# Kernel tuning notes

Measured on AMD Instinct MI355X. Metric: run time of the kernel, lower is better.

Reference implementation:

```python
import jax, jax.numpy as jnp
import numpy as np


def setup_inputs() -> dict:
    key = jax.random.key(0)
    k1, k2 = jax.random.split(key)
    B, C, H, W = 32, 8, 256, 256
    inp = jax.random.normal(k1, (B, C, H, W), dtype=jnp.float32)
    tgt = jax.random.uniform(k2, (B, C, H, W), dtype=jnp.float32)
    return {"input": inp, "target": tgt}


def reference(input, target):
    B, C, H, W = input.shape
    # normalized coordinate grids: (index+1)/size, as in the original loops
    x_grid = (jnp.arange(W, dtype=input.dtype) + 1.0) / W          # [W]
    y_grid = (jnp.arange(H, dtype=input.dtype) + 1.0) / H          # [H]

    # per-(b,c) softmax over the flattened heatmap (DSNT)
    p = jax.nn.softmax(input.reshape(B, C, H * W), axis=-1).reshape(B, C, H, W)
    pred_x = jnp.einsum('bchw,w->bc', p, x_grid)                   # [B, C]
    pred_y = jnp.einsum('bchw,h->bc', p, y_grid)                   # [B, C]

    # ground-truth coords from argmax of target heatmap
    idx = jnp.argmax(target.reshape(B, C, H * W), axis=-1)         # [B, C] int
    true_x = ((idx % W) + 1).astype(input.dtype) / W
    true_y = ((idx // W) + 1).astype(input.dtype) / H

    ed = jnp.sqrt((true_x - pred_x) ** 2 + (true_y - pred_y) ** 2)  # [B, C]
    # original sums over all (batch, channel) pairs, divides by batch size only
    return jnp.sum(ed) / B
```

## Files before the change

### kernel.cpp

```cpp
#include <hip/hip_runtime.h>
#include <math.h>


constexpr int HW    = 256 * 256;
constexpr int BLOCK = 1024;
constexpr int WAVES = BLOCK / 64;
constexpr int ITERS = (HW / 4) / BLOCK;

__global__ __launch_bounds__(BLOCK) void dsnt_loss_kernel(
        const float* __restrict__ input,
        const float* __restrict__ target,
        float* __restrict__ out)
{
    const int bc = blockIdx.x;
    const float4* __restrict__ in4 =
        reinterpret_cast<const float4*>(input) + (size_t)bc * (HW / 4);
    const float4* __restrict__ tg4 =
        reinterpret_cast<const float4*>(target) + (size_t)bc * (HW / 4);
    const int tid = threadIdx.x;

    float s = 0.f, sx = 0.f, sy = 0.f;
    float bv = -INFINITY;
    int   bi = 0x7FFFFFFF;

    #pragma unroll
    for (int i = 0; i < ITERS; ++i) {
        const int j = tid + i * BLOCK;
        const float4 v = in4[j];
        const float4 t = tg4[j];
        const int f = 4 * j;
        const float y  = (float)((f >> 8) + 1) * (1.0f / 256.0f);
        const float x0 = (float)((f & 255) + 1) * (1.0f / 256.0f);

        const float e0 = __expf(v.x);
        const float e1 = __expf(v.y);
        const float e2 = __expf(v.z);
        const float e3 = __expf(v.w);
        const float es = (e0 + e1) + (e2 + e3);
        s  += es;
        sy += es * y;
        sx += e0 * x0
            + e1 * (x0 + 1.0f / 256.0f)
            + e2 * (x0 + 2.0f / 256.0f)
            + e3 * (x0 + 3.0f / 256.0f);

        if (t.x > bv) { bv = t.x; bi = f; }
        if (t.y > bv) { bv = t.y; bi = f + 1; }
        if (t.z > bv) { bv = t.z; bi = f + 2; }
        if (t.w > bv) { bv = t.w; bi = f + 3; }
    }

    #pragma unroll
    for (int off = 32; off > 0; off >>= 1) {
        s  += __shfl_down(s, off);
        sx += __shfl_down(sx, off);
        sy += __shfl_down(sy, off);
        const float ov = __shfl_down(bv, off);
        const int   oi = __shfl_down(bi, off);
        if (ov > bv || (ov == bv && oi < bi)) { bv = ov; bi = oi; }
    }

    __shared__ float ls[WAVES], lsx[WAVES], lsy[WAVES], lbv[WAVES];
    __shared__ int   lbi[WAVES];
    const int wave = tid >> 6;
    const int lane = tid & 63;
    if (lane == 0) {
        ls[wave]  = s;
        lsx[wave] = sx;
        lsy[wave] = sy;
        lbv[wave] = bv;
        lbi[wave] = bi;
    }
    __syncthreads();

    if (tid == 0) {
        #pragma unroll
        for (int wv = 1; wv < WAVES; ++wv) {
            s  += ls[wv];
            sx += lsx[wv];
            sy += lsy[wv];
            if (lbv[wv] > bv || (lbv[wv] == bv && lbi[wv] < bi)) {
                bv = lbv[wv];
                bi = lbi[wv];
            }
        }
        const float px = sx / s;
        const float py = sy / s;
        const float tx = (float)((bi & 255) + 1) * (1.0f / 256.0f);
        const float ty = (float)((bi >> 8) + 1) * (1.0f / 256.0f);
        const float dx = tx - px;
        const float dy = ty - py;
        const float ed = sqrtf(dx * dx + dy * dy);
        atomicAdd(out, ed * (1.0f / 32.0f));
    }
}

extern "C" void kernel_launch(void* const* d_in, const int* in_sizes, int n_in,
                              void* d_out, int out_size, void* d_ws, size_t ws_size,
                              hipStream_t stream) {
    const float* input  = (const float*)d_in[0];
    const float* target = (const float*)d_in[1];
    float* out = (float*)d_out;

    const int n_maps = in_sizes[0] / HW;

    hipMemsetAsync(out, 0, sizeof(float), stream);
    dsnt_loss_kernel<<<n_maps, BLOCK, 0, stream>>>(input, target, out);
}
```

Measured before the change: 146.6 us.

## Split each heatmap across multiple blocks with atomic partial reduction and final kernel

Each (b,c) map is now processed by 8 blocks of 512 threads instead of one 1024-thread block, giving 2048 blocks rather than 256 so the 256 CUs fill more evenly and more loads stay in flight. Partial sums go to a workspace through float atomics, and the argmax is merged with a packed 64-bit atomicMax key that breaks ties toward the lower index. A second small kernel finishes the per-map loss and the sum. This adds a memset, a second launch and atomic traffic, and float atomics make the sum order nondeterministic.

```diff
diff --git a/kernel.cpp b/kernel.cpp
--- a/kernel.cpp
+++ b/kernel.cpp
@@ -2,22 +2,33 @@
 #include <math.h>
 
 
-constexpr int HW    = 256 * 256;
-constexpr int BLOCK = 1024;
-constexpr int WAVES = BLOCK / 64;
-constexpr int ITERS = (HW / 4) / BLOCK;
+constexpr int HW     = 256 * 256;
+constexpr int SPLIT  = 8;
+constexpr int BLOCK  = 512;
+constexpr int WAVES  = BLOCK / 64;
+constexpr int CHUNK4 = (HW / 4) / SPLIT;
+constexpr int ITERS  = CHUNK4 / BLOCK;
 
-__global__ __launch_bounds__(BLOCK) void dsnt_loss_kernel(
+struct Ws {
+    unsigned long long key[256];
+    float s[256];
+    float sx[256];
+    float sy[256];
+};
+
+__global__ __launch_bounds__(BLOCK) void dsnt_partial_kernel(
         const float* __restrict__ input,
         const float* __restrict__ target,
-        float* __restrict__ out)
+        Ws* __restrict__ ws)
 {
-    const int bc = blockIdx.x;
-    const float4* __restrict__ in4 =
-        reinterpret_cast<const float4*>(input) + (size_t)bc * (HW / 4);
-    const float4* __restrict__ tg4 =
-        reinterpret_cast<const float4*>(target) + (size_t)bc * (HW / 4);
-    const int tid = threadIdx.x;
+    const int chunk = blockIdx.x;
+    const int bc    = blockIdx.y;
+    const int tid   = threadIdx.x;
+
+    const size_t base4 = (size_t)bc * (HW / 4) + (size_t)chunk * CHUNK4;
+    const float4* __restrict__ in4 = reinterpret_cast<const float4*>(input)  + base4;
+    const float4* __restrict__ tg4 = reinterpret_cast<const float4*>(target) + base4;
+    const int fbase = chunk * (HW / SPLIT);
 
     float s = 0.f, sx = 0.f, sy = 0.f;
     float bv = -INFINITY;
@@ -28,7 +39,7 @@
         const int j = tid + i * BLOCK;
         const float4 v = in4[j];
         const float4 t = tg4[j];
-        const int f = 4 * j;
+        const int f = fbase + 4 * j;
         const float y  = (float)((f >> 8) + 1) * (1.0f / 256.0f);
         const float x0 = (float)((f & 255) + 1) * (1.0f / 256.0f);
 
@@ -65,11 +76,8 @@
     const int wave = tid >> 6;
     const int lane = tid & 63;
     if (lane == 0) {
-        ls[wave]  = s;
-        lsx[wave] = sx;
-        lsy[wave] = sy;
-        lbv[wave] = bv;
-        lbi[wave] = bi;
+        ls[wave] = s; lsx[wave] = sx; lsy[wave] = sy;
+        lbv[wave] = bv; lbi[wave] = bi;
     }
     __syncthreads();
 
@@ -80,18 +88,46 @@
             sx += lsx[wv];
             sy += lsy[wv];
             if (lbv[wv] > bv || (lbv[wv] == bv && lbi[wv] < bi)) {
-                bv = lbv[wv];
-                bi = lbi[wv];
+                bv = lbv[wv]; bi = lbi[wv];
             }
         }
-        const float px = sx / s;
-        const float py = sy / s;
+        atomicAdd(&ws->s[bc],  s);
+        atomicAdd(&ws->sx[bc], sx);
+        atomicAdd(&ws->sy[bc], sy);
+        const unsigned long long key =
+            ((unsigned long long)__float_as_uint(bv) << 32) |
+            (unsigned long long)(~(unsigned int)bi);
+        atomicMax(&ws->key[bc], key);
+    }
+}
+
+__global__ __launch_bounds__(256) void dsnt_final_kernel(
+        const Ws* __restrict__ ws,
+        float* __restrict__ out,
+        int n_maps)
+{
+    const int tid = threadIdx.x;
+    float ed = 0.f;
+    if (tid < n_maps) {
+        const float s  = ws->s[tid];
+        const float px = ws->sx[tid] / s;
+        const float py = ws->sy[tid] / s;
+        const unsigned int inv_idx = (unsigned int)(ws->key[tid] & 0xFFFFFFFFu);
+        const int bi = (int)(~inv_idx);
         const float tx = (float)((bi & 255) + 1) * (1.0f / 256.0f);
         const float ty = (float)((bi >> 8) + 1) * (1.0f / 256.0f);
         const float dx = tx - px;
         const float dy = ty - py;
-        const float ed = sqrtf(dx * dx + dy * dy);
-        atomicAdd(out, ed * (1.0f / 32.0f));
+        ed = sqrtf(dx * dx + dy * dy);
+    }
+    #pragma unroll
+    for (int off = 32; off > 0; off >>= 1) ed += __shfl_down(ed, off);
+    __shared__ float lw[4];
+    const int wave = tid >> 6;
+    if ((tid & 63) == 0) lw[wave] = ed;
+    __syncthreads();
+    if (tid == 0) {
+        out[0] = (lw[0] + lw[1] + lw[2] + lw[3]) * (1.0f / 32.0f);
     }
 }
 
@@ -101,9 +137,11 @@
     const float* input  = (const float*)d_in[0];
     const float* target = (const float*)d_in[1];
     float* out = (float*)d_out;
+    Ws* ws = (Ws*)d_ws;
 
     const int n_maps = in_sizes[0] / HW;
 
-    hipMemsetAsync(out, 0, sizeof(float), stream);
-    dsnt_loss_kernel<<<n_maps, BLOCK, 0, stream>>>(input, target, out);
+    hipMemsetAsync(ws, 0, sizeof(Ws), stream);
+    dsnt_partial_kernel<<<dim3(SPLIT, n_maps), BLOCK, 0, stream>>>(input, target, ws);
+    dsnt_final_kernel<<<1, 256, 0, stream>>>(ws, out, n_maps);
 }
```

Result: no change. 147.3 us (+0.5%).
